# Kernel tuning notes

Hardware: AMD Instinct MI355X
Metric: run time of the kernel (lower is better)

Reference implementation:

```python
import jax, jax.numpy as jnp
import numpy as np

N, E, G = 100000, 600000, 2000
CONV = [128, 256, 256, 256]
LIN = [256, 128, 1]
BN_EPS = 1e-5


def setup_inputs() -> dict:
    key = jax.random.key(0)
    ks = iter(jax.random.split(key, 64))
    inp = {}
    inp["x"] = jax.random.normal(next(ks), (N, CONV[0]), dtype=jnp.float32)
    inp["edge_index"] = jax.random.randint(next(ks), (2, E), 0, N)
    inp["batch"] = jnp.sort(jax.random.randint(next(ks), (N,), 0, G))

    def lin_w(k, i, o):
        return (jax.random.normal(k, (i, o), dtype=jnp.float32) / np.sqrt(i)).astype(jnp.float32)

    # 3 GINConv MLPs: Linear(in,out), BN(out), ReLU, Linear(out,out), ReLU
    for i in range(3):
        ci, co = CONV[i], CONV[i + 1]
        inp[f"c{i}_w1"] = lin_w(next(ks), ci, co)
        inp[f"c{i}_b1"] = jnp.zeros((co,), jnp.float32)
        inp[f"c{i}_g"] = jnp.ones((co,), jnp.float32)
        inp[f"c{i}_be"] = jnp.zeros((co,), jnp.float32)
        inp[f"c{i}_m"] = jax.random.normal(next(ks), (co,), dtype=jnp.float32) * 0.1
        inp[f"c{i}_v"] = jax.random.uniform(next(ks), (co,), minval=0.5, maxval=1.5, dtype=jnp.float32)
        inp[f"c{i}_w2"] = lin_w(next(ks), co, co)
        inp[f"c{i}_b2"] = jnp.zeros((co,), jnp.float32)
    # head: Linear(256,128) + BN(128) + ReLU, Linear(128,1)
    inp["l0_w"] = lin_w(next(ks), LIN[0], LIN[1])
    inp["l0_b"] = jnp.zeros((LIN[1],), jnp.float32)
    inp["l0_g"] = jnp.ones((LIN[1],), jnp.float32)
    inp["l0_be"] = jnp.zeros((LIN[1],), jnp.float32)
    inp["l0_m"] = jax.random.normal(next(ks), (LIN[1],), dtype=jnp.float32) * 0.1
    inp["l0_v"] = jax.random.uniform(next(ks), (LIN[1],), minval=0.5, maxval=1.5, dtype=jnp.float32)
    inp["l1_w"] = lin_w(next(ks), LIN[1], LIN[2])
    inp["l1_b"] = jnp.zeros((LIN[2],), jnp.float32)
    return inp


def _bn(h, g, be, m, v):
    return g * (h - m) * jax.lax.rsqrt(v + BN_EPS) + be


def _gin_conv(x, src, dst, w1, b1, g, be, m, v, w2, b2):
    # GINConv (eps=0): MLP(x + sum_{j in N(i)} x_j); messages x[src] aggregated at dst
    agg = jax.ops.segment_sum(x[src], dst, num_segments=x.shape[0])
    h = (x + agg) @ w1 + b1
    h = jax.nn.relu(_bn(h, g, be, m, v))
    return jax.nn.relu(h @ w2 + b2)


def reference(x, edge_index, batch,
              c0_w1, c0_b1, c0_g, c0_be, c0_m, c0_v, c0_w2, c0_b2,
              c1_w1, c1_b1, c1_g, c1_be, c1_m, c1_v, c1_w2, c1_b2,
              c2_w1, c2_b1, c2_g, c2_be, c2_m, c2_v, c2_w2, c2_b2,
              l0_w, l0_b, l0_g, l0_be, l0_m, l0_v, l1_w, l1_b):
    src, dst = edge_index[0], edge_index[1]
    conv_params = [
        (c0_w1, c0_b1, c0_g, c0_be, c0_m, c0_v, c0_w2, c0_b2),
        (c1_w1, c1_b1, c1_g, c1_be, c1_m, c1_v, c1_w2, c1_b2),
        (c2_w1, c2_b1, c2_g, c2_be, c2_m, c2_v, c2_w2, c2_b2),
    ]
    h = x
    for i, p in enumerate(conv_params):
        h = _gin_conv(h, src, dst, *p)
        if i < 2:
            h = jax.nn.relu(h)  # outer activation (no-op after ReLU, kept for fidelity)
    # global_add_pool over graphs
    h = jax.ops.segment_sum(h, batch, num_segments=G)  # [G, 256]
    h = h @ l0_w + l0_b
    h = _bn(h, l0_g, l0_be, l0_m, l0_v)
    h = jax.nn.relu(h)  # dropout is identity in eval mode
    return h @ l1_w + l1_b  # [G, 1]
```

## Files before the change

kernel.cpp:

```cpp
#include <hip/hip_runtime.h>
#include <hip/hip_bf16.h>

#define BN_EPS 1e-5f

typedef __attribute__((ext_vector_type(8))) short short8;
typedef __attribute__((ext_vector_type(4))) float f32x4;

__device__ __forceinline__ void gll16(const void* g, void* l) {
    __builtin_amdgcn_global_load_lds(
        (const __attribute__((address_space(1))) unsigned int*)g,
        (__attribute__((address_space(3))) unsigned int*)l, 16, 0, 0);
}

__global__ void hist_kernel(const int* __restrict__ dst, int* __restrict__ off, int E) {
    int e = blockIdx.x * blockDim.x + threadIdx.x;
    if (e < E) atomicAdd(&off[dst[e] + 1], 1);
}

__global__ __launch_bounds__(256) void scan1_kernel(int* __restrict__ data,
                                                    int* __restrict__ sums, int n) {
    __shared__ int sh[256];
    const int t = threadIdx.x;
    const int idx = blockIdx.x * 1024 + t * 4;
    int v[4];
    int s = 0;
#pragma unroll
    for (int j = 0; j < 4; ++j) {
        int x = (idx + j < n) ? data[idx + j] : 0;
        s += x;
        v[j] = s;
    }
    sh[t] = s;
    __syncthreads();
    for (int o = 1; o < 256; o <<= 1) {
        int x = (t >= o) ? sh[t - o] : 0;
        __syncthreads();
        sh[t] += x;
        __syncthreads();
    }
    const int prev = sh[t] - s;
#pragma unroll
    for (int j = 0; j < 4; ++j) {
        if (idx + j < n) data[idx + j] = v[j] + prev;
    }
    if (t == 255) sums[blockIdx.x] = sh[255];
}

__global__ __launch_bounds__(256) void scan2_kernel(int* __restrict__ sums, int nb) {
    __shared__ int sh[256];
    const int t = threadIdx.x;
    sh[t] = (t < nb) ? sums[t] : 0;
    __syncthreads();
    for (int o = 1; o < 256; o <<= 1) {
        int x = (t >= o) ? sh[t - o] : 0;
        __syncthreads();
        sh[t] += x;
        __syncthreads();
    }
    if (t < nb) sums[t] = sh[t];
}

__global__ void scan3_kernel(int* __restrict__ data, const int* __restrict__ sums,
                             int* __restrict__ cursor, int n, int N) {
    int i = blockIdx.x * blockDim.x + threadIdx.x;
    if (i >= n) return;
    int b = i >> 10;
    int v = data[i];
    if (b > 0) { v += sums[b - 1]; data[i] = v; }
    if (i < N) cursor[i] = v;
}

__global__ void fill_kernel(const int* __restrict__ src, const int* __restrict__ dst,
                            int* __restrict__ cursor, int* __restrict__ sorted_src, int E) {
    int e = blockIdx.x * blockDim.x + threadIdx.x;
    if (e >= E) return;
    int p = atomicAdd(&cursor[dst[e]], 1);
    sorted_src[p] = src[e];
}

__global__ void cvt_x_kernel(const float* __restrict__ x, __hip_bfloat16* __restrict__ xb,
                             int N, int total ) {
    int i = blockIdx.x * blockDim.x + threadIdx.x;
    if (i >= total) return;
    int n = i >> 7;
    float v = (n < N) ? x[i] : 0.f;
    xb[i] = __float2bfloat16(v);
}

__global__ void wt_all_kernel(const float* __restrict__ w0, const float* __restrict__ w1,
                              const float* __restrict__ w2, const float* __restrict__ w3,
                              const float* __restrict__ w4, const float* __restrict__ w5,
                              __hip_bfloat16* __restrict__ o0, __hip_bfloat16* __restrict__ o1,
                              __hip_bfloat16* __restrict__ o2, __hip_bfloat16* __restrict__ o3,
                              __hip_bfloat16* __restrict__ o4, __hip_bfloat16* __restrict__ o5) {
    int i = blockIdx.x * blockDim.x + threadIdx.x;
    const int S0 = 256 * 128, S = 256 * 256;
    if (i < S0) {
        int m = i / 128, k = i - m * 128;
        o0[i] = __float2bfloat16(w0[k * 256 + m]);
        return;
    }
    i -= S0;
    int mi = i / S, j = i - mi * S;
    if (mi >= 5) return;
    int m = j >> 8, k = j & 255;
    const float* Wp; __hip_bfloat16* Op;
    switch (mi) {
        case 0: Wp = w1; Op = o1; break;
        case 1: Wp = w2; Op = o2; break;
        case 2: Wp = w3; Op = o3; break;
        case 3: Wp = w4; Op = o4; break;
        default: Wp = w5; Op = o5; break;
    }
    Op[j] = __float2bfloat16(Wp[k * 256 + m]);
}

__global__ void prep_ss_kernel(
    const float* __restrict__ g0, const float* __restrict__ be0, const float* __restrict__ m0,
    const float* __restrict__ v0, const float* __restrict__ b10, const float* __restrict__ b20,
    const float* __restrict__ g1, const float* __restrict__ be1, const float* __restrict__ m1,
    const float* __restrict__ v1, const float* __restrict__ b11, const float* __restrict__ b21,
    const float* __restrict__ g2, const float* __restrict__ be2, const float* __restrict__ m2,
    const float* __restrict__ v2, const float* __restrict__ b12, const float* __restrict__ b22,
    float* __restrict__ ss) {
    const int layer = blockIdx.x;
    const int c = threadIdx.x;
    const float *g, *be, *m, *v, *b1, *b2;
    switch (layer) {
        case 0: g = g0; be = be0; m = m0; v = v0; b1 = b10; b2 = b20; break;
        case 1: g = g1; be = be1; m = m1; v = v1; b1 = b11; b2 = b21; break;
        default: g = g2; be = be2; m = m2; v = v2; b1 = b12; b2 = b22; break;
    }
    float r = rsqrtf(v[c] + BN_EPS);
    float s = g[c] * r;
    ss[(2 * layer) * 512 + c] = s;
    ss[(2 * layer) * 512 + 256 + c] = (b1[c] - m[c]) * s + be[c];
    ss[(2 * layer + 1) * 512 + c] = 1.f;
    ss[(2 * layer + 1) * 512 + 256 + c] = b2[c];
}

template <int C>
__global__ __launch_bounds__(256) void agg_fused(const __hip_bfloat16* __restrict__ h,
                                                 const int* __restrict__ off,
                                                 const int* __restrict__ ssrc,
                                                 __hip_bfloat16* __restrict__ out, int N) {
    constexpr int L = C / 8;
    int t = blockIdx.x * blockDim.x + threadIdx.x;
    int n = t / L;
    if (n >= N) return;
    int c8 = t - n * L;
    const uint4* hp = (const uint4*)h;

    float acc[8];
    {
        uint4 sv = hp[(size_t)n * L + c8];
        const unsigned u[4] = {sv.x, sv.y, sv.z, sv.w};
#pragma unroll
        for (int j = 0; j < 4; ++j) {
            acc[2 * j]     = __uint_as_float(u[j] << 16);
            acc[2 * j + 1] = __uint_as_float(u[j] & 0xffff0000u);
        }
    }
    const int e0 = off[n], e1 = off[n + 1];
    int e = e0;
    for (; e + 2 <= e1; e += 2) {
        int s0 = ssrc[e], s1 = ssrc[e + 1];
        uint4 a = hp[(size_t)s0 * L + c8];
        uint4 b = hp[(size_t)s1 * L + c8];
        const unsigned ua[4] = {a.x, a.y, a.z, a.w};
        const unsigned ub[4] = {b.x, b.y, b.z, b.w};
#pragma unroll
        for (int j = 0; j < 4; ++j) {
            acc[2 * j]     += __uint_as_float(ua[j] << 16);
            acc[2 * j + 1] += __uint_as_float(ua[j] & 0xffff0000u);
            acc[2 * j]     += __uint_as_float(ub[j] << 16);
            acc[2 * j + 1] += __uint_as_float(ub[j] & 0xffff0000u);
        }
    }
    if (e < e1) {
        int s0 = ssrc[e];
        uint4 a = hp[(size_t)s0 * L + c8];
        const unsigned ua[4] = {a.x, a.y, a.z, a.w};
#pragma unroll
        for (int j = 0; j < 4; ++j) {
            acc[2 * j]     += __uint_as_float(ua[j] << 16);
            acc[2 * j + 1] += __uint_as_float(ua[j] & 0xffff0000u);
        }
    }
    unsigned o[4];
#pragma unroll
    for (int j = 0; j < 4; ++j) {
        __hip_bfloat16 a = __float2bfloat16(acc[2 * j]);
        __hip_bfloat16 b = __float2bfloat16(acc[2 * j + 1]);
        unsigned short ua = *(unsigned short*)&a, ub = *(unsigned short*)&b;
        o[j] = (unsigned)ua | ((unsigned)ub << 16);
    }
    ((uint4*)out)[(size_t)n * L + c8] = make_uint4(o[0], o[1], o[2], o[3]);
}

template <int K>
__global__ __launch_bounds__(256) void gemm_mfma(
    const __hip_bfloat16* __restrict__ A,
    const __hip_bfloat16* __restrict__ Wt,
    const float* __restrict__ sc, const float* __restrict__ sh,
    __hip_bfloat16* __restrict__ C) {
    __shared__ short ldsA[2][128 * 64];
    __shared__ short ldsB[2][128 * 64];

    const int tid = threadIdx.x;
    const int l = tid & 63;
    const int w = tid >> 6;
    const int wr = w >> 1, wc = w & 1;
    const int rb = blockIdx.x >> 1;
    const int cb = blockIdx.x & 1;
    const int row0 = rb * 128;
    const int col0 = cb * 128;

    f32x4 acc[4][4] = {};

    const int swz_st = ((l & 7) * 16) ^ ((l >> 3) << 4);
    const char* Ab = (const char*)A + (size_t)(row0 + w * 32 + (l >> 3)) * (K * 2) + swz_st;
    const char* Bb = (const char*)Wt + (size_t)(col0 + w * 32 + (l >> 3)) * (K * 2) + swz_st;

    const int fr_row = l & 15;
    const int fr_sl = (l >> 4) * 16;
    const int fr_x = (l & 7) << 4;

    constexpr int NT = K / 64;

    auto stage = [&](int buf, int t) {
#pragma unroll
        for (int i = 0; i < 4; ++i) {
            gll16(Ab + (size_t)t * 128 + (size_t)(i * 8) * (K * 2),
                  (char*)&ldsA[buf][0] + (w * 32 + i * 8) * 128);
            gll16(Bb + (size_t)t * 128 + (size_t)(i * 8) * (K * 2),
                  (char*)&ldsB[buf][0] + (w * 32 + i * 8) * 128);
        }
    };

    stage(0, 0);
    asm volatile("s_waitcnt vmcnt(0)" ::: "memory");
    __builtin_amdgcn_s_barrier();

    int cur = 0;
#pragma unroll
    for (int t = 0; t < NT; ++t) {
        if (t + 1 < NT) stage(cur ^ 1, t + 1);

#pragma unroll
        for (int k0 = 0; k0 < 2; ++k0) {
            short8 af[4], bf[4];
            const int byt = (k0 * 64 + fr_sl) ^ fr_x;
#pragma unroll
            for (int mi = 0; mi < 4; ++mi) {
                int row = wr * 64 + mi * 16 + fr_row;
                af[mi] = *(const short8*)((const char*)&ldsA[cur][0] + row * 128 + byt);
            }
#pragma unroll
            for (int ni = 0; ni < 4; ++ni) {
                int col = wc * 64 + ni * 16 + fr_row;
                bf[ni] = *(const short8*)((const char*)&ldsB[cur][0] + col * 128 + byt);
            }
#pragma unroll
            for (int mi = 0; mi < 4; ++mi)
#pragma unroll
                for (int ni = 0; ni < 4; ++ni)
                    acc[mi][ni] = __builtin_amdgcn_mfma_f32_16x16x32_bf16(
                        af[mi], bf[ni], acc[mi][ni], 0, 0, 0);
        }

        if (t + 1 < NT) {
            asm volatile("s_waitcnt vmcnt(0)" ::: "memory");
            __builtin_amdgcn_s_barrier();
            cur ^= 1;
        }
    }

    const int lr = l >> 4;
    const int lc = l & 15;
#pragma unroll
    for (int ni = 0; ni < 4; ++ni) {
        const int col = col0 + wc * 64 + ni * 16 + lc;
        const float s = sc[col], t = sh[col];
#pragma unroll
        for (int mi = 0; mi < 4; ++mi) {
            const int grow = row0 + wr * 64 + mi * 16 + lr * 4;
#pragma unroll
            for (int r = 0; r < 4; ++r) {
                float vv = acc[mi][ni][r] * s + t;
                vv = fmaxf(vv, 0.f);
                C[(size_t)(grow + r) * 256 + col] = __float2bfloat16(vv);
            }
        }
    }
}

__device__ __forceinline__ int lower_bound_dev(const int* __restrict__ a, int n, int key) {
    int lo = 0, hi = n;
    while (lo < hi) {
        int mid = (lo + hi) >> 1;
        if (a[mid] < key) lo = mid + 1; else hi = mid;
    }
    return lo;
}

__global__ __launch_bounds__(256) void pool_seg_kernel(const __hip_bfloat16* __restrict__ h,
                                                       const int* __restrict__ batch,
                                                       float* __restrict__ pooled, int N) {
    __shared__ int seg[2];
    const int g = blockIdx.x;
    if (threadIdx.x == 0) seg[0] = lower_bound_dev(batch, N, g);
    if (threadIdx.x == 1) seg[1] = lower_bound_dev(batch, N, g + 1);
    __syncthreads();
    const int c = threadIdx.x;
    float acc = 0.f;
    for (int n = seg[0]; n < seg[1]; ++n) acc += __bfloat162float(h[(size_t)n * 256 + c]);
    pooled[(size_t)g * 256 + c] = acc;
}

__global__ __launch_bounds__(128) void head_kernel(
    const float* __restrict__ pooled,
    const float* __restrict__ w0, const float* __restrict__ b0,
    const float* __restrict__ g, const float* __restrict__ be,
    const float* __restrict__ m, const float* __restrict__ v,
    const float* __restrict__ w1, const float* __restrict__ b1,
    float* __restrict__ out) {
    __shared__ float row[256];
    __shared__ float red[128];
    const int gid = blockIdx.x;
    const int j = threadIdx.x;

    row[j]       = pooled[(size_t)gid * 256 + j];
    row[j + 128] = pooled[(size_t)gid * 256 + 128 + j];
    __syncthreads();

    float acc = b0[j];
#pragma unroll 8
    for (int k = 0; k < 256; ++k) acc += row[k] * w0[k * 128 + j];

    float h = g[j] * (acc - m[j]) * rsqrtf(v[j] + BN_EPS) + be[j];
    h = fmaxf(h, 0.f) * w1[j];
    red[j] = h;
    __syncthreads();
    for (int s = 64; s > 0; s >>= 1) {
        if (j < s) red[j] += red[j + s];
        __syncthreads();
    }
    if (j == 0) out[gid] = red[0] + b1[0];
}

extern "C" void kernel_launch(void* const* d_in, const int* in_sizes, int n_in,
                              void* d_out, int out_size, void* d_ws, size_t ws_size,
                              hipStream_t stream) {
    const float* x    = (const float*)d_in[0];
    const int* eidx   = (const int*)d_in[1];
    const int* batch  = (const int*)d_in[2];

    const int N = in_sizes[0] / 128;
    const int E = in_sizes[1] / 2;
    const int G = out_size;

    const int* src = eidx;
    const int* dst = eidx + E;

    const float* cw1[3]; const float* cb1[3]; const float* cg[3]; const float* cbe[3];
    const float* cm[3];  const float* cv[3];  const float* cw2[3]; const float* cb2[3];
    for (int i = 0; i < 3; ++i) {
        int b = 3 + i * 8;
        cw1[i] = (const float*)d_in[b + 0];
        cb1[i] = (const float*)d_in[b + 1];
        cg[i]  = (const float*)d_in[b + 2];
        cbe[i] = (const float*)d_in[b + 3];
        cm[i]  = (const float*)d_in[b + 4];
        cv[i]  = (const float*)d_in[b + 5];
        cw2[i] = (const float*)d_in[b + 6];
        cb2[i] = (const float*)d_in[b + 7];
    }
    const float* l0_w  = (const float*)d_in[27];
    const float* l0_b  = (const float*)d_in[28];
    const float* l0_g  = (const float*)d_in[29];
    const float* l0_be = (const float*)d_in[30];
    const float* l0_m  = (const float*)d_in[31];
    const float* l0_v  = (const float*)d_in[32];
    const float* l1_w  = (const float*)d_in[33];
    const float* l1_b  = (const float*)d_in[34];

    float* outp = (float*)d_out;

    const int nrb  = (N + 127) / 128;
    const int Npad = nrb * 128;
    const size_t SB = (size_t)Npad * 256 * 2;
    const size_t XB = (size_t)Npad * 128 * 2;
    const size_t PB = (size_t)G * 256 * 4;
    const size_t WTB = (size_t)256 * 256 * 2;

    char* ws = (char*)d_ws;
    size_t o = 0;
    __hip_bfloat16* B1 = (__hip_bfloat16*)(ws + o); o += SB;
    __hip_bfloat16* B2 = (__hip_bfloat16*)(ws + o); o += SB;
    __hip_bfloat16* B3 = (__hip_bfloat16*)(ws + o); o += SB;
    __hip_bfloat16* xb = (__hip_bfloat16*)(ws + o); o += XB;
    float* pooled      = (float*)(ws + o);       o += PB;
    __hip_bfloat16* wt[6];
    for (int i = 0; i < 6; ++i) { wt[i] = (__hip_bfloat16*)(ws + o); o += WTB; }
    float* ss          = (float*)(ws + o);       o += 6 * 512 * 4;
    int* csr_off    = (int*)(ws + o); o += (size_t)(N + 1) * 4;
    int* cursor     = (int*)(ws + o); o += (size_t)N * 4;
    int* sorted_src = (int*)(ws + o); o += (size_t)E * 4;
    int* sums       = (int*)(ws + o); o += 256 * 4;
    if (ws_size < o) return;

    const dim3 blk(256);

    {
        int total = Npad * 128;
        cvt_x_kernel<<<(total + 255) / 256, blk, 0, stream>>>(x, xb, N, total);
    }
    {
        int total = 256 * 128 + 5 * 256 * 256;
        wt_all_kernel<<<(total + 255) / 256, blk, 0, stream>>>(
            cw1[0], cw2[0], cw1[1], cw2[1], cw1[2], cw2[2],
            wt[0], wt[1], wt[2], wt[3], wt[4], wt[5]);
    }
    prep_ss_kernel<<<3, blk, 0, stream>>>(
        cg[0], cbe[0], cm[0], cv[0], cb1[0], cb2[0],
        cg[1], cbe[1], cm[1], cv[1], cb1[1], cb2[1],
        cg[2], cbe[2], cm[2], cv[2], cb1[2], cb2[2], ss);

    {
        const int n_off = N + 1;
        hipMemsetAsync(csr_off, 0, (size_t)n_off * sizeof(int), stream);
        hist_kernel<<<(E + 255) / 256, blk, 0, stream>>>(dst, csr_off, E);
        const int nb = (n_off + 1023) / 1024;
        scan1_kernel<<<nb, blk, 0, stream>>>(csr_off, sums, n_off);
        scan2_kernel<<<1, blk, 0, stream>>>(sums, nb);
        scan3_kernel<<<(n_off + 255) / 256, blk, 0, stream>>>(csr_off, sums, cursor, n_off, N);
        fill_kernel<<<(E + 255) / 256, blk, 0, stream>>>(src, dst, cursor, sorted_src, E);
    }

    const int gemm_grid = nrb * 2;
    auto SC = [&](int i) { return ss + i * 512; };
    auto SH = [&](int i) { return ss + i * 512 + 256; };

    {
        int total = N * 16;
        agg_fused<128><<<(total + 255) / 256, blk, 0, stream>>>(xb, csr_off, sorted_src, B1, N);
    }
    gemm_mfma<128><<<gemm_grid, blk, 0, stream>>>(B1, wt[0], SC(0), SH(0), B2);
    gemm_mfma<256><<<gemm_grid, blk, 0, stream>>>(B2, wt[1], SC(1), SH(1), B3);

    {
        int total = N * 32;
        agg_fused<256><<<(total + 255) / 256, blk, 0, stream>>>(B3, csr_off, sorted_src, B1, N);
    }
    gemm_mfma<256><<<gemm_grid, blk, 0, stream>>>(B1, wt[2], SC(2), SH(2), B2);
    gemm_mfma<256><<<gemm_grid, blk, 0, stream>>>(B2, wt[3], SC(3), SH(3), B3);

    {
        int total = N * 32;
        agg_fused<256><<<(total + 255) / 256, blk, 0, stream>>>(B3, csr_off, sorted_src, B1, N);
    }
    gemm_mfma<256><<<gemm_grid, blk, 0, stream>>>(B1, wt[4], SC(4), SH(4), B2);
    gemm_mfma<256><<<gemm_grid, blk, 0, stream>>>(B2, wt[5], SC(5), SH(5), B3);

    pool_seg_kernel<<<G, blk, 0, stream>>>(B3, batch, pooled, N);
    head_kernel<<<G, dim3(128), 0, stream>>>(pooled, l0_w, l0_b, l0_g, l0_be, l0_m, l0_v,
                                             l1_w, l1_b, outp);
}
```

Baseline: 460.1 us.

## Fuse both GEMMs of each GIN MLP into one kernel with LDS-resident intermediate

Replaces the pair of per-layer GEMM launches with a single 512-thread kernel. Each block loads a 128-row tile of the aggregated input into LDS, computes the first linear+BN+ReLU, writes that intermediate back into LDS as bf16, then runs the second GEMM against double-buffered weight tiles. This removes the global-memory round trip of the intermediate activation and halves the number of GEMM launches. Each block now covers all 256 output columns, so there are half as many blocks and each uses a large LDS footprint (about 128KB), which lowers occupancy. The second and third layers write their output in place into their input buffer, which is safe only because each block reads its own rows before writing them.

```diff
diff --git a/kernel.cpp b/kernel.cpp
--- a/kernel.cpp
+++ b/kernel.cpp
@@ -10,6 +10,12 @@
     __builtin_amdgcn_global_load_lds(
         (const __attribute__((address_space(1))) unsigned int*)g,
         (__attribute__((address_space(3))) unsigned int*)l, 16, 0, 0);
+}
+
+__device__ __forceinline__ unsigned pack_bf2(float a, float b) {
+    __hip_bfloat16 ba = __float2bfloat16(a);
+    __hip_bfloat16 bb = __float2bfloat16(b);
+    return (unsigned)(*(unsigned short*)&ba) | ((unsigned)(*(unsigned short*)&bb) << 16);
 }
 
 __global__ void hist_kernel(const int* __restrict__ dst, int* __restrict__ off, int E) {
@@ -189,107 +195,139 @@
     }
     unsigned o[4];
 #pragma unroll
-    for (int j = 0; j < 4; ++j) {
-        __hip_bfloat16 a = __float2bfloat16(acc[2 * j]);
-        __hip_bfloat16 b = __float2bfloat16(acc[2 * j + 1]);
-        unsigned short ua = *(unsigned short*)&a, ub = *(unsigned short*)&b;
-        o[j] = (unsigned)ua | ((unsigned)ub << 16);
-    }
+    for (int j = 0; j < 4; ++j) o[j] = pack_bf2(acc[2 * j], acc[2 * j + 1]);
     ((uint4*)out)[(size_t)n * L + c8] = make_uint4(o[0], o[1], o[2], o[3]);
 }
 
-template <int K>
-__global__ __launch_bounds__(256) void gemm_mfma(
+template <int K1>
+__global__ __launch_bounds__(512) void mlp_fused(
     const __hip_bfloat16* __restrict__ A,
-    const __hip_bfloat16* __restrict__ Wt,
-    const float* __restrict__ sc, const float* __restrict__ sh,
+    const __hip_bfloat16* __restrict__ W1t,
+    const __hip_bfloat16* __restrict__ W2t,
+    const float* __restrict__ ss1, const float* __restrict__ ss2,
     __hip_bfloat16* __restrict__ C) {
-    __shared__ short ldsA[2][128 * 64];
-    __shared__ short ldsB[2][128 * 64];
+    __shared__ __align__(16) char bufAT[64 * 1024];
+    __shared__ __align__(16) char bufW[2][32 * 1024];
 
     const int tid = threadIdx.x;
-    const int l = tid & 63;
-    const int w = tid >> 6;
-    const int wr = w >> 1, wc = w & 1;
-    const int rb = blockIdx.x >> 1;
-    const int cb = blockIdx.x & 1;
-    const int row0 = rb * 128;
-    const int col0 = cb * 128;
-
-    f32x4 acc[4][4] = {};
-
-    const int swz_st = ((l & 7) * 16) ^ ((l >> 3) << 4);
-    const char* Ab = (const char*)A + (size_t)(row0 + w * 32 + (l >> 3)) * (K * 2) + swz_st;
-    const char* Bb = (const char*)Wt + (size_t)(col0 + w * 32 + (l >> 3)) * (K * 2) + swz_st;
-
-    const int fr_row = l & 15;
-    const int fr_sl = (l >> 4) * 16;
-    const int fr_x = (l & 7) << 4;
-
-    constexpr int NT = K / 64;
-
-    auto stage = [&](int buf, int t) {
-#pragma unroll
-        for (int i = 0; i < 4; ++i) {
-            gll16(Ab + (size_t)t * 128 + (size_t)(i * 8) * (K * 2),
-                  (char*)&ldsA[buf][0] + (w * 32 + i * 8) * 128);
-            gll16(Bb + (size_t)t * 128 + (size_t)(i * 8) * (K * 2),
-                  (char*)&ldsB[buf][0] + (w * 32 + i * 8) * 128);
+    const int l   = tid & 63;
+    const int w   = tid >> 6;
+    const int wr  = w >> 2;
+    const int wc  = w & 3;
+    const size_t row0 = (size_t)blockIdx.x * 128;
+
+    constexpr int ROWB = K1 * 2;
+    constexpr int NT1  = K1 / 64;
+    constexpr int NIA  = 128 * ROWB / 1024;
+    constexpr int RPI  = 1024 / ROWB;
+
+    const int lswz = (l & 7) << 4;
+
+    {
+        const char* Ab = (const char*)(A + row0 * K1);
+#pragma unroll
+        for (int i = w; i < NIA; i += 8) {
+            int row = i * RPI + (l * 16) / ROWB;
+            int byt = ((l * 16) % ROWB) ^ ((row & 7) << 4);
+            gll16(Ab + (size_t)row * ROWB + byt, bufAT + i * 1024);
+        }
+    }
+    auto stageW = [&](const __hip_bfloat16* Wsrc, int Krow2, int t, int buf) {
+        const char* Wb = (const char*)Wsrc;
+#pragma unroll
+        for (int i = w; i < 32; i += 8) {
+            int c = i * 8 + (l >> 3);
+            int byt = ((l & 7) * 16) ^ ((c & 7) << 4);
+            gll16(Wb + (size_t)c * Krow2 + t * 128 + byt, bufW[buf] + i * 1024);
         }
     };
-
-    stage(0, 0);
-    asm volatile("s_waitcnt vmcnt(0)" ::: "memory");
-    __builtin_amdgcn_s_barrier();
-
-    int cur = 0;
-#pragma unroll
-    for (int t = 0; t < NT; ++t) {
-        if (t + 1 < NT) stage(cur ^ 1, t + 1);
-
+    stageW(W1t, ROWB, 0, 0);
+    __syncthreads();
+
+    f32x4 acc1[4][4] = {};
+    int buf = 0;
+#pragma unroll
+    for (int t = 0; t < NT1; ++t) {
+        if (t + 1 < NT1) stageW(W1t, ROWB, t + 1, buf ^ 1);
+        else             stageW(W2t, 512, 0, buf ^ 1);
 #pragma unroll
         for (int k0 = 0; k0 < 2; ++k0) {
-            short8 af[4], bf[4];
-            const int byt = (k0 * 64 + fr_sl) ^ fr_x;
-#pragma unroll
-            for (int mi = 0; mi < 4; ++mi) {
-                int row = wr * 64 + mi * 16 + fr_row;
-                af[mi] = *(const short8*)((const char*)&ldsA[cur][0] + row * 128 + byt);
+            short8 wf[4], af[4];
+            const int wbyt = (k0 * 64 + (l >> 4) * 16) ^ lswz;
+            const int abyt = (t * 128 + k0 * 64 + (l >> 4) * 16) ^ lswz;
+#pragma unroll
+            for (int i = 0; i < 4; ++i) {
+                const int c = wc * 64 + i * 16 + (l & 15);
+                wf[i] = *(const short8*)(bufW[buf] + c * 128 + wbyt);
+                const int r = wr * 64 + i * 16 + (l & 15);
+                af[i] = *(const short8*)(bufAT + r * ROWB + abyt);
             }
 #pragma unroll
-            for (int ni = 0; ni < 4; ++ni) {
-                int col = wc * 64 + ni * 16 + fr_row;
-                bf[ni] = *(const short8*)((const char*)&ldsB[cur][0] + col * 128 + byt);
+            for (int mi = 0; mi < 4; ++mi)
+#pragma unroll
+                for (int nj = 0; nj < 4; ++nj)
+                    acc1[mi][nj] = __builtin_amdgcn_mfma_f32_16x16x32_bf16(
+                        wf[mi], af[nj], acc1[mi][nj], 0, 0, 0);
+        }
+        __syncthreads();
+        buf ^= 1;
+    }
+
+#pragma unroll
+    for (int mi = 0; mi < 4; ++mi) {
+        const int m0 = wc * 64 + mi * 16 + (l >> 4) * 4;
+        const float4 s4 = *(const float4*)(ss1 + m0);
+        const float4 h4 = *(const float4*)(ss1 + 256 + m0);
+        const int byt = (m0 * 2) ^ lswz;
+#pragma unroll
+        for (int nj = 0; nj < 4; ++nj) {
+            const int n = wr * 64 + nj * 16 + (l & 15);
+            const float v0 = fmaxf(acc1[mi][nj][0] * s4.x + h4.x, 0.f);
+            const float v1 = fmaxf(acc1[mi][nj][1] * s4.y + h4.y, 0.f);
+            const float v2 = fmaxf(acc1[mi][nj][2] * s4.z + h4.z, 0.f);
+            const float v3 = fmaxf(acc1[mi][nj][3] * s4.w + h4.w, 0.f);
+            *(uint2*)(bufAT + n * 512 + byt) = make_uint2(pack_bf2(v0, v1), pack_bf2(v2, v3));
+        }
+    }
+    __syncthreads();
+
+    f32x4 acc2[4][4] = {};
+#pragma unroll
+    for (int s = 0; s < 4; ++s) {
+        if (s < 3) stageW(W2t, 512, s + 1, buf ^ 1);
+#pragma unroll
+        for (int k0 = 0; k0 < 2; ++k0) {
+            short8 tf[4], wf[4];
+            const int tbyt = (s * 128 + k0 * 64 + (l >> 4) * 16) ^ lswz;
+            const int wbyt = (k0 * 64 + (l >> 4) * 16) ^ lswz;
+#pragma unroll
+            for (int i = 0; i < 4; ++i) {
+                const int r = wr * 64 + i * 16 + (l & 15);
+                tf[i] = *(const short8*)(bufAT + r * 512 + tbyt);
+                const int c = wc * 64 + i * 16 + (l & 15);
+                wf[i] = *(const short8*)(bufW[buf] + c * 128 + wbyt);
             }
 #pragma unroll
             for (int mi = 0; mi < 4; ++mi)
 #pragma unroll
                 for (int ni = 0; ni < 4; ++ni)
-                    acc[mi][ni] = __builtin_amdgcn_mfma_f32_16x16x32_bf16(
-                        af[mi], bf[ni], acc[mi][ni], 0, 0, 0);
-        }
-
-        if (t + 1 < NT) {
-            asm volatile("s_waitcnt vmcnt(0)" ::: "memory");
-            __builtin_amdgcn_s_barrier();
-            cur ^= 1;
-        }
-    }
-
-    const int lr = l >> 4;
-    const int lc = l & 15;
+                    acc2[mi][ni] = __builtin_amdgcn_mfma_f32_16x16x32_bf16(
+                        tf[mi], wf[ni], acc2[mi][ni], 0, 0, 0);
+        }
+        if (s < 3) { __syncthreads(); buf ^= 1; }
+    }
+
 #pragma unroll
     for (int ni = 0; ni < 4; ++ni) {
-        const int col = col0 + wc * 64 + ni * 16 + lc;
-        const float s = sc[col], t = sh[col];
+        const int col = wc * 64 + ni * 16 + (l & 15);
+        const float sc = ss2[col], sh = ss2[256 + col];
 #pragma unroll
         for (int mi = 0; mi < 4; ++mi) {
-            const int grow = row0 + wr * 64 + mi * 16 + lr * 4;
+            const size_t grow = row0 + wr * 64 + mi * 16 + (l >> 4) * 4;
 #pragma unroll
             for (int r = 0; r < 4; ++r) {
-                float vv = acc[mi][ni][r] * s + t;
-                vv = fmaxf(vv, 0.f);
-                C[(size_t)(grow + r) * 256 + col] = __float2bfloat16(vv);
+                float vv = fmaxf(acc2[mi][ni][r] * sc + sh, 0.f);
+                C[(grow + r) * 256 + col] = __float2bfloat16(vv);
             }
         }
     }
@@ -396,9 +434,8 @@
 
     char* ws = (char*)d_ws;
     size_t o = 0;
-    __hip_bfloat16* B1 = (__hip_bfloat16*)(ws + o); o += SB;
-    __hip_bfloat16* B2 = (__hip_bfloat16*)(ws + o); o += SB;
-    __hip_bfloat16* B3 = (__hip_bfloat16*)(ws + o); o += SB;
+    __hip_bfloat16* U  = (__hip_bfloat16*)(ws + o); o += SB;
+    __hip_bfloat16* V  = (__hip_bfloat16*)(ws + o); o += SB;
     __hip_bfloat16* xb = (__hip_bfloat16*)(ws + o); o += XB;
     float* pooled      = (float*)(ws + o);       o += PB;
     __hip_bfloat16* wt[6];
@@ -438,32 +475,27 @@
         fill_kernel<<<(E + 255) / 256, blk, 0, stream>>>(src, dst, cursor, sorted_src, E);
     }
 
-    const int gemm_grid = nrb * 2;
-    auto SC = [&](int i) { return ss + i * 512; };
-    auto SH = [&](int i) { return ss + i * 512 + 256; };
+    auto SS = [&](int i) { return ss + i * 512; };
 
     {
         int total = N * 16;
-        agg_fused<128><<<(total + 255) / 256, blk, 0, stream>>>(xb, csr_off, sorted_src, B1, N);
-    }
-    gemm_mfma<128><<<gemm_grid, blk, 0, stream>>>(B1, wt[0], SC(0), SH(0), B2);
-    gemm_mfma<256><<<gemm_grid, blk, 0, stream>>>(B2, wt[1], SC(1), SH(1), B3);
+        agg_fused<128><<<(total + 255) / 256, blk, 0, stream>>>(xb, csr_off, sorted_src, U, N);
+    }
+    mlp_fused<128><<<nrb, dim3(512), 0, stream>>>(U, wt[0], wt[1], SS(0), SS(1), V);
 
     {
         int total = N * 32;
-        agg_fused<256><<<(total + 255) / 256, blk, 0, stream>>>(B3, csr_off, sorted_src, B1, N);
-    }
-    gemm_mfma<256><<<gemm_grid, blk, 0, stream>>>(B1, wt[2], SC(2), SH(2), B2);
-    gemm_mfma<256><<<gemm_grid, blk, 0, stream>>>(B2, wt[3], SC(3), SH(3), B3);
+        agg_fused<256><<<(total + 255) / 256, blk, 0, stream>>>(V, csr_off, sorted_src, U, N);
+    }
+    mlp_fused<256><<<nrb, dim3(512), 0, stream>>>(U, wt[2], wt[3], SS(2), SS(3), U);
 
     {
         int total = N * 32;
-        agg_fused<256><<<(total + 255) / 256, blk, 0, stream>>>(B3, csr_off, sorted_src, B1, N);
-    }
-    gemm_mfma<256><<<gemm_grid, blk, 0, stream>>>(B1, wt[4], SC(4), SH(4), B2);
-    gemm_mfma<256><<<gemm_grid, blk, 0, stream>>>(B2, wt[5], SC(5), SH(5), B3);
-
-    pool_seg_kernel<<<G, blk, 0, stream>>>(B3, batch, pooled, N);
+        agg_fused<256><<<(total + 255) / 256, blk, 0, stream>>>(U, csr_off, sorted_src, V, N);
+    }
+    mlp_fused<256><<<nrb, dim3(512), 0, stream>>>(V, wt[4], wt[5], SS(4), SS(5), V);
+
+    pool_seg_kernel<<<G, blk, 0, stream>>>(V, batch, pooled, N);
     head_kernel<<<G, dim3(128), 0, stream>>>(pooled, l0_w, l0_b, l0_g, l0_be, l0_m, l0_v,
                                              l1_w, l1_b, outp);
 }
```

Measured after the change: 437.1 us. 1.05x faster.
